# Kernel optimization log

Measured on AMD Instinct MI355X. Metric: run time of the kernel, lower is better.

## Reference

```python
import jax, jax.numpy as jnp
import numpy as np

B, C, T = 2, 128, 25000
OUT_C = 128
N_NODES = B * T            # 50000, nodes after flatten
N_EDGES = 800000           # avg degree 16


def setup_inputs() -> dict:
    key = jax.random.key(0)
    k1, k2, k3 = jax.random.split(key, 3)
    x = jax.random.normal(k1, (B, C, T), dtype=jnp.float32)
    W = jax.random.normal(k2, (C, OUT_C), dtype=jnp.float32) * (1.0 / np.sqrt(C))
    bias = jnp.zeros((OUT_C,), dtype=jnp.float32)
    edge_index = jax.random.randint(k3, (2, N_EDGES), 0, N_NODES, dtype=jnp.int64)
    return {"x": x, "W": W, "bias": bias, "edge_index": edge_index}


def reference(x, W, bias, edge_index):
    b, c, t = x.shape
    n = b * t
    flat = x.transpose(0, 2, 1).reshape(n, c)          # [N, C]
    h = flat @ W                                       # [N, OUT_C] transform first (GCNConv)
    src, dst = edge_index[0], edge_index[1]
    # in-degree with self-loops (PyG GCNConv default symmetric norm)
    deg = jnp.zeros((n,), dtype=h.dtype).at[dst].add(1.0) + 1.0
    dinv_sqrt = jax.lax.rsqrt(deg)
    norm = dinv_sqrt[src] * dinv_sqrt[dst]             # [E]
    msgs = h[src] * norm[:, None]                      # [E, OUT_C] gather + scale
    agg = jax.ops.segment_sum(msgs, dst, num_segments=n)
    agg = agg + h * (1.0 / deg)[:, None]               # self-loop term: norm_ii = 1/deg_i
    out = jax.nn.relu(agg + bias)
    return out.reshape(b, t, -1).transpose(0, 2, 1)    # [B, OUT_C, T]
```

## Files before the change

### kernel.cpp

```cpp
#include <hip/hip_runtime.h>

#define TT 25000
#define BB 2
#define CC 128
#define NN (BB*TT)
#define GEMMB ((NN + 63) / 64)
#define CAP 64

typedef __attribute__((ext_vector_type(8))) short bf16x8;
typedef __attribute__((ext_vector_type(4))) float f32x4;

__device__ inline unsigned short f2bf(float f) {
    unsigned int u = __float_as_uint(f);
    u += 0x7FFF + ((u >> 16) & 1);
    return (unsigned short)(u >> 16);
}
__device__ inline float bfhi(unsigned int v) { return __uint_as_float(v << 16); }
__device__ inline float bflo(unsigned int v) { return __uint_as_float(v & 0xFFFF0000u); }

__global__ __launch_bounds__(256) void k_dg(const float* __restrict__ x,
                                            const float* __restrict__ W,
                                            unsigned short* __restrict__ h,
                                            const int* __restrict__ src,
                                            const int* __restrict__ dst, int E,
                                            int* __restrict__ deg,
                                            int* __restrict__ csr) {
    __shared__ __align__(16) unsigned short a_lds[4][4][64][8];
    __shared__ __align__(16) unsigned short b_lds[8][4][64][8];
    int role = (blockIdx.x >> 3) & 1;
    int idx  = ((blockIdx.x >> 4) << 3) | (blockIdx.x & 7);
    int tid = threadIdx.x;

    if (role) {
        int db = (E + 1023) >> 10;
        if (idx >= db) return;
        int base = idx * 1024 + tid;
#pragma unroll
        for (int u = 0; u < 4; ++u) {
            int i = base + u * 256;
            if (i < E) {
                int d = dst[i];
                int e = atomicAdd(&deg[d], 1);
                if (e < CAP)
                    csr[(size_t)d * CAP + e] = src[i];
            }
        }
        return;
    }

    if (idx >= GEMMB) return;
    int n0 = idx * 64;

    {
        int m = tid & 63;
        int n = n0 + m;
        bool ok = (n < NN);
        int b = 0, t = 0;
        if (ok) { b = n / TT; t = n - b * TT; }
        const float* xp = x + ((size_t)b * CC) * TT + t;
        int mt = m >> 4, lm = m & 15;
#pragma unroll
        for (int p = 0; p < 4; ++p) {
            int kg = (tid >> 6) + p * 4;
            unsigned short tmp[8];
#pragma unroll
            for (int j = 0; j < 8; ++j) {
                float v = ok ? xp[(size_t)(kg * 8 + j) * TT] : 0.f;
                tmp[j] = f2bf(v);
            }
            int kk = kg >> 2, q = kg & 3;
            *(bf16x8*)&a_lds[mt][kk][lm | (q << 4)][0] = *(bf16x8*)tmp;
        }
    }
    {
        int nc = tid & 127;
        int nt = nc >> 4, ln = nc & 15;
#pragma unroll
        for (int p = 0; p < 8; ++p) {
            int kg = (tid >> 7) + p * 2;
            unsigned short tmp[8];
#pragma unroll
            for (int j = 0; j < 8; ++j)
                tmp[j] = f2bf(W[(kg * 8 + j) * CC + nc]);
            int kk = kg >> 2, q = kg & 3;
            *(bf16x8*)&b_lds[nt][kk][ln | (q << 4)][0] = *(bf16x8*)tmp;
        }
    }
    __syncthreads();

    int lane = tid & 63;
    int w = tid >> 6;
    f32x4 acc[8];
#pragma unroll
    for (int nt = 0; nt < 8; ++nt) acc[nt] = (f32x4){0.f, 0.f, 0.f, 0.f};
#pragma unroll
    for (int kk = 0; kk < 4; ++kk) {
        bf16x8 a = *(const bf16x8*)&a_lds[w][kk][lane][0];
#pragma unroll
        for (int nt = 0; nt < 8; ++nt) {
            bf16x8 bb = *(const bf16x8*)&b_lds[nt][kk][lane][0];
            acc[nt] = __builtin_amdgcn_mfma_f32_16x16x32_bf16(a, bb, acc[nt], 0, 0, 0);
        }
    }

    int q = lane >> 4, col = lane & 15;
    int nodebase = n0 + w * 16 + q * 4;
#pragma unroll
    for (int nt = 0; nt < 8; ++nt) {
#pragma unroll
        for (int r = 0; r < 4; ++r) {
            int nn = nodebase + r;
            if (nn < NN)
                h[(size_t)nn * CC + nt * 16 + col] = f2bf(acc[nt][r]);
        }
    }
}

__global__ __launch_bounds__(256) void k_dinv(const int* __restrict__ deg,
                                              float* __restrict__ dinv) {
    int i = blockIdx.x * 256 + threadIdx.x;
    if (i < NN) dinv[i] = rsqrtf((float)(deg[i] + 1));
}

__global__ __launch_bounds__(512) void k_aggt(const unsigned int* __restrict__ hb,
                                              const int* __restrict__ deg,
                                              const int* __restrict__ csr,
                                              const float* __restrict__ dinv,
                                              const float* __restrict__ bias,
                                              float* __restrict__ out) {
    __shared__ float tile[32][129];
    int lane = threadIdx.x & 63;
    int w    = threadIdx.x >> 6;
    int n0   = blockIdx.x * 32;
    const float2 bb = ((const float2*)bias)[lane];

#pragma unroll
    for (int r = 0; r < 4; ++r) {
        int lt = w * 4 + r;
        int un = __builtin_amdgcn_readfirstlane(n0 + lt);
        if (un < NN) {
            int dg  = deg[un];
            int cnt = dg < CAP ? dg : CAP;
            float dn = rsqrtf((float)(dg + 1));
            const int* row = csr + (size_t)un * CAP;
            float ax = 0.f, ay = 0.f;

            int j = 0;
            for (; j + 8 <= cnt; j += 8) {
                int s[8];
#pragma unroll
                for (int u = 0; u < 8; ++u) s[u] = row[j + u];
                float dv[8];
#pragma unroll
                for (int u = 0; u < 8; ++u) dv[u] = dinv[s[u]];
                unsigned int v[8];
#pragma unroll
                for (int u = 0; u < 8; ++u) v[u] = hb[(size_t)s[u] * 64 + lane];
#pragma unroll
                for (int u = 0; u < 8; ++u) {
                    ax = fmaf(dv[u], bfhi(v[u]), ax);
                    ay = fmaf(dv[u], bflo(v[u]), ay);
                }
            }
            for (; j < cnt; ++j) {
                int s = row[j];
                float dv = dinv[s];
                unsigned int v = hb[(size_t)s * 64 + lane];
                ax = fmaf(dv, bfhi(v), ax);
                ay = fmaf(dv, bflo(v), ay);
            }

            unsigned int hv = hb[(size_t)un * 64 + lane];
            ax = fmaf(dn, bfhi(hv), ax);
            ay = fmaf(dn, bflo(hv), ay);
            float rx = fmaxf(fmaf(dn, ax, bb.x), 0.f);
            float ry = fmaxf(fmaf(dn, ay, bb.y), 0.f);
            tile[lt][2 * lane]     = rx;
            tile[lt][2 * lane + 1] = ry;
        }
    }
    __syncthreads();

    int tx = threadIdx.x & 31;
    int cg = threadIdx.x >> 5;
    int n = n0 + tx;
    if (n < NN) {
        int b = n / TT, t = n - b * TT;
#pragma unroll
        for (int i = 0; i < 8; ++i) {
            int ch = cg + i * 16;
            out[((size_t)b * CC + ch) * TT + t] = tile[tx][ch];
        }
    }
}

extern "C" void kernel_launch(void* const* d_in, const int* in_sizes, int n_in,
                              void* d_out, int out_size, void* d_ws, size_t ws_size,
                              hipStream_t stream) {
    const float* x    = (const float*)d_in[0];
    const float* W    = (const float*)d_in[1];
    const float* bias = (const float*)d_in[2];
    const int*   ei   = (const int*)d_in[3];
    int E = in_sizes[3] / 2;
    const int* src = ei;
    const int* dst = ei + E;
    float* out = (float*)d_out;

    char* ws = (char*)d_ws;
    size_t o = 0;
    unsigned short* h = (unsigned short*)(ws + o); o += (size_t)NN * CC * 2;
    int*   deg  = (int*)  (ws + o); o += (size_t)NN * 4;
    float* dinv = (float*)(ws + o); o += (size_t)NN * 4;
    int*   csr  = (int*)  (ws + o); o += (size_t)NN * CAP * 4;

    hipMemsetAsync(deg, 0, (size_t)NN * 4, stream);

    int db = (E + 1023) / 1024;
    int mx = (GEMMB > db) ? GEMMB : db;
    int grid = 2 * ((mx + 7) / 8) * 8;
    k_dg  <<<grid, 256, 0, stream>>>(x, W, h, src, dst, E, deg, csr);
    k_dinv<<<(NN + 255) / 256, 256, 0, stream>>>(deg, dinv);
    k_aggt<<<(NN + 31) / 32, 512, 0, stream>>>((const unsigned int*)h, deg, csr, dinv, bias, out);
}
```

Baseline: 164.2 us.

## Merge memset, GEMM/CSR build and dinv into one persistent cooperative kernel

Replaces the memset, the combined GEMM/degree kernel and the dinv kernel with a single cooperative persistent kernel. It zeroes deg, runs a grid sync, loops over GEMM tiles and edge chunks with a grid-stride, syncs the grid again, and then computes dinv. This removes two launches and the memset at the cost of two grid-wide barriers and fewer resident blocks (up to 3 per CU times 256). The smaller grid may leave less parallelism for the atomic-heavy CSR build and for the strided x loads.

```diff
diff --git a/kernel.cpp b/kernel.cpp
--- a/kernel.cpp
+++ b/kernel.cpp
@@ -1,4 +1,6 @@
 #include <hip/hip_runtime.h>
+#include <hip/hip_cooperative_groups.h>
+namespace cg = cooperative_groups;
 
 #define TT 25000
 #define BB 2
@@ -18,108 +20,116 @@
 __device__ inline float bfhi(unsigned int v) { return __uint_as_float(v << 16); }
 __device__ inline float bflo(unsigned int v) { return __uint_as_float(v & 0xFFFF0000u); }
 
-__global__ __launch_bounds__(256) void k_dg(const float* __restrict__ x,
-                                            const float* __restrict__ W,
-                                            unsigned short* __restrict__ h,
-                                            const int* __restrict__ src,
-                                            const int* __restrict__ dst, int E,
-                                            int* __restrict__ deg,
-                                            int* __restrict__ csr) {
+__global__ __launch_bounds__(256) void k_main(const float* __restrict__ x,
+                                              const float* __restrict__ W,
+                                              unsigned short* __restrict__ h,
+                                              const int* __restrict__ src,
+                                              const int* __restrict__ dst, int E,
+                                              int* __restrict__ deg,
+                                              int* __restrict__ csr,
+                                              float* __restrict__ dinv) {
     __shared__ __align__(16) unsigned short a_lds[4][4][64][8];
     __shared__ __align__(16) unsigned short b_lds[8][4][64][8];
+    cg::grid_group grid = cg::this_grid();
+    int tid = threadIdx.x;
+    int nth = (int)gridDim.x * 256;
+    int gt  = (int)blockIdx.x * 256 + tid;
+
+    for (int i = gt; i < NN; i += nth) deg[i] = 0;
+    grid.sync();
+
     int role = (blockIdx.x >> 3) & 1;
-    int idx  = ((blockIdx.x >> 4) << 3) | (blockIdx.x & 7);
-    int tid = threadIdx.x;
+    int rb   = (int)gridDim.x >> 1;
+    int ridx = (int)(((blockIdx.x >> 4) << 3) | (blockIdx.x & 7));
 
     if (role) {
         int db = (E + 1023) >> 10;
-        if (idx >= db) return;
-        int base = idx * 1024 + tid;
-#pragma unroll
-        for (int u = 0; u < 4; ++u) {
-            int i = base + u * 256;
-            if (i < E) {
-                int d = dst[i];
-                int e = atomicAdd(&deg[d], 1);
-                if (e < CAP)
-                    csr[(size_t)d * CAP + e] = src[i];
-            }
-        }
-        return;
-    }
-
-    if (idx >= GEMMB) return;
-    int n0 = idx * 64;
-
-    {
-        int m = tid & 63;
-        int n = n0 + m;
-        bool ok = (n < NN);
-        int b = 0, t = 0;
-        if (ok) { b = n / TT; t = n - b * TT; }
-        const float* xp = x + ((size_t)b * CC) * TT + t;
-        int mt = m >> 4, lm = m & 15;
-#pragma unroll
-        for (int p = 0; p < 4; ++p) {
-            int kg = (tid >> 6) + p * 4;
-            unsigned short tmp[8];
-#pragma unroll
-            for (int j = 0; j < 8; ++j) {
-                float v = ok ? xp[(size_t)(kg * 8 + j) * TT] : 0.f;
-                tmp[j] = f2bf(v);
-            }
-            int kk = kg >> 2, q = kg & 3;
-            *(bf16x8*)&a_lds[mt][kk][lm | (q << 4)][0] = *(bf16x8*)tmp;
-        }
-    }
-    {
-        int nc = tid & 127;
-        int nt = nc >> 4, ln = nc & 15;
-#pragma unroll
-        for (int p = 0; p < 8; ++p) {
-            int kg = (tid >> 7) + p * 2;
-            unsigned short tmp[8];
-#pragma unroll
-            for (int j = 0; j < 8; ++j)
-                tmp[j] = f2bf(W[(kg * 8 + j) * CC + nc]);
-            int kk = kg >> 2, q = kg & 3;
-            *(bf16x8*)&b_lds[nt][kk][ln | (q << 4)][0] = *(bf16x8*)tmp;
-        }
-    }
-    __syncthreads();
-
-    int lane = tid & 63;
-    int w = tid >> 6;
-    f32x4 acc[8];
-#pragma unroll
-    for (int nt = 0; nt < 8; ++nt) acc[nt] = (f32x4){0.f, 0.f, 0.f, 0.f};
-#pragma unroll
-    for (int kk = 0; kk < 4; ++kk) {
-        bf16x8 a = *(const bf16x8*)&a_lds[w][kk][lane][0];
-#pragma unroll
-        for (int nt = 0; nt < 8; ++nt) {
-            bf16x8 bb = *(const bf16x8*)&b_lds[nt][kk][lane][0];
-            acc[nt] = __builtin_amdgcn_mfma_f32_16x16x32_bf16(a, bb, acc[nt], 0, 0, 0);
-        }
-    }
-
-    int q = lane >> 4, col = lane & 15;
-    int nodebase = n0 + w * 16 + q * 4;
-#pragma unroll
-    for (int nt = 0; nt < 8; ++nt) {
-#pragma unroll
-        for (int r = 0; r < 4; ++r) {
-            int nn = nodebase + r;
-            if (nn < NN)
-                h[(size_t)nn * CC + nt * 16 + col] = f2bf(acc[nt][r]);
-        }
-    }
-}
-
-__global__ __launch_bounds__(256) void k_dinv(const int* __restrict__ deg,
-                                              float* __restrict__ dinv) {
-    int i = blockIdx.x * 256 + threadIdx.x;
-    if (i < NN) dinv[i] = rsqrtf((float)(deg[i] + 1));
+        for (int c = ridx; c < db; c += rb) {
+            int base = c * 1024 + tid;
+#pragma unroll
+            for (int u = 0; u < 4; ++u) {
+                int i = base + u * 256;
+                if (i < E) {
+                    int d = dst[i];
+                    int e = atomicAdd(&deg[d], 1);
+                    if (e < CAP)
+                        csr[(size_t)d * CAP + e] = src[i];
+                }
+            }
+        }
+    } else {
+        for (int tile = ridx; tile < GEMMB; tile += rb) {
+            int n0 = tile * 64;
+
+            {
+                int m = tid & 63;
+                int n = n0 + m;
+                bool ok = (n < NN);
+                int b = 0, t = 0;
+                if (ok) { b = n / TT; t = n - b * TT; }
+                const float* xp = x + ((size_t)b * CC) * TT + t;
+                int mt = m >> 4, lm = m & 15;
+#pragma unroll
+                for (int p = 0; p < 4; ++p) {
+                    int kg = (tid >> 6) + p * 4;
+                    unsigned short tmp[8];
+#pragma unroll
+                    for (int j = 0; j < 8; ++j) {
+                        float v = ok ? xp[(size_t)(kg * 8 + j) * TT] : 0.f;
+                        tmp[j] = f2bf(v);
+                    }
+                    int kk = kg >> 2, q = kg & 3;
+                    *(bf16x8*)&a_lds[mt][kk][lm | (q << 4)][0] = *(bf16x8*)tmp;
+                }
+            }
+            {
+                int nc = tid & 127;
+                int nt = nc >> 4, ln = nc & 15;
+#pragma unroll
+                for (int p = 0; p < 8; ++p) {
+                    int kg = (tid >> 7) + p * 2;
+                    unsigned short tmp[8];
+#pragma unroll
+                    for (int j = 0; j < 8; ++j)
+                        tmp[j] = f2bf(W[(kg * 8 + j) * CC + nc]);
+                    int kk = kg >> 2, q = kg & 3;
+                    *(bf16x8*)&b_lds[nt][kk][ln | (q << 4)][0] = *(bf16x8*)tmp;
+                }
+            }
+            __syncthreads();
+
+            int lane = tid & 63;
+            int w = tid >> 6;
+            f32x4 acc[8];
+#pragma unroll
+            for (int nt = 0; nt < 8; ++nt) acc[nt] = (f32x4){0.f, 0.f, 0.f, 0.f};
+#pragma unroll
+            for (int kk = 0; kk < 4; ++kk) {
+                bf16x8 a = *(const bf16x8*)&a_lds[w][kk][lane][0];
+#pragma unroll
+                for (int nt = 0; nt < 8; ++nt) {
+                    bf16x8 bb = *(const bf16x8*)&b_lds[nt][kk][lane][0];
+                    acc[nt] = __builtin_amdgcn_mfma_f32_16x16x32_bf16(a, bb, acc[nt], 0, 0, 0);
+                }
+            }
+
+            int q = lane >> 4, col = lane & 15;
+            int nodebase = n0 + w * 16 + q * 4;
+#pragma unroll
+            for (int nt = 0; nt < 8; ++nt) {
+#pragma unroll
+                for (int r = 0; r < 4; ++r) {
+                    int nn = nodebase + r;
+                    if (nn < NN)
+                        h[(size_t)nn * CC + nt * 16 + col] = f2bf(acc[nt][r]);
+                }
+            }
+            __syncthreads();
+        }
+    }
+    grid.sync();
+
+    for (int i = gt; i < NN; i += nth) dinv[i] = rsqrtf((float)(deg[i] + 1));
 }
 
 __global__ __launch_bounds__(512) void k_aggt(const unsigned int* __restrict__ hb,
@@ -182,13 +192,13 @@
     __syncthreads();
 
     int tx = threadIdx.x & 31;
-    int cg = threadIdx.x >> 5;
+    int cg_ = threadIdx.x >> 5;
     int n = n0 + tx;
     if (n < NN) {
         int b = n / TT, t = n - b * TT;
 #pragma unroll
         for (int i = 0; i < 8; ++i) {
-            int ch = cg + i * 16;
+            int ch = cg_ + i * 16;
             out[((size_t)b * CC + ch) * TT + t] = tile[tx][ch];
         }
     }
@@ -213,12 +223,21 @@
     float* dinv = (float*)(ws + o); o += (size_t)NN * 4;
     int*   csr  = (int*)  (ws + o); o += (size_t)NN * CAP * 4;
 
-    hipMemsetAsync(deg, 0, (size_t)NN * 4, stream);
-
-    int db = (E + 1023) / 1024;
-    int mx = (GEMMB > db) ? GEMMB : db;
-    int grid = 2 * ((mx + 7) / 8) * 8;
-    k_dg  <<<grid, 256, 0, stream>>>(x, W, h, src, dst, E, deg, csr);
-    k_dinv<<<(NN + 255) / 256, 256, 0, stream>>>(deg, dinv);
-    k_aggt<<<(NN + 31) / 32, 512, 0, stream>>>((const unsigned int*)h, deg, csr, dinv, bias, out);
-}
+    static int nbpc = 0;
+    if (nbpc == 0) {
+        int q = 0;
+        hipError_t err = hipOccupancyMaxActiveBlocksPerMultiprocessor(
+            &q, reinterpret_cast<const void*>(k_main), 256, 0);
+        nbpc = (err == hipSuccess && q >= 1) ? q : 2;
+        if (nbpc > 3) nbpc = 3;
+    }
+    int grid = nbpc * 256;
+
+    void* args[] = {(void*)&x, (void*)&W, (void*)&h, (void*)&src, (void*)&dst,
+                    (void*)&E, (void*)&deg, (void*)&csr, (void*)&dinv};
+    hipLaunchCooperativeKernel(reinterpret_cast<const void*>(k_main),
+                               dim3(grid), dim3(256), args, 0, stream);
+
+    k_aggt<<<(NN + 31) / 32, 512, 0, stream>>>((const unsigned int*)h, deg, csr,
+                                               dinv, bias, out);
+}
```

Result: slower. 228.8 us (+39.3%).
